# Kernel optimization log

Hardware: AMD Instinct MI355X
Metric: run time of the kernel (lower is better)

Reference implementation:

```python
import jax, jax.numpy as jnp
import numpy as np

B, N0, C, K, D = 16384, 1024, 12, 64, 3  # batch, feat dim, num_classes, num_clusters, ndim


def setup_inputs() -> dict:
    key = jax.random.key(0)
    ks = jax.random.split(key, 6)
    s = 0.02  # weight init scale
    return {
        "x": jax.random.normal(ks[0], (B, N0), dtype=jnp.float32),
        "Wfc": jax.random.normal(ks[1], (N0, C), dtype=jnp.float32) * s,
        "bfc": jnp.zeros((C,), dtype=jnp.float32),
        "Wbin": jax.random.normal(ks[2], (C, K, N0), dtype=jnp.float32) * s,
        "bbin": jnp.zeros((C, K), dtype=jnp.float32),
        "Wres": jax.random.normal(ks[3], (C, K, N0, D), dtype=jnp.float32) * s,
        "bres": jnp.zeros((C, K, D), dtype=jnp.float32),
        "centers": jax.random.normal(ks[4], (K, D), dtype=jnp.float32),
    }


def reference(x, Wfc, bfc, Wbin, bbin, Wres, bres, centers):
    # category head
    y0 = x @ Wfc + bfc                                            # [B, C]
    # per-class bin logits (batched over all classes at once)
    ybin = jnp.einsum("bn,ckn->bck", x, Wbin) + bbin              # [B, C, K]
    ind = jnp.argmax(ybin, axis=2)                                # [B, C] selected cluster per class
    # multires path: all (class, cluster) expert residuals, then one-hot select
    yres_all = jnp.einsum("bn,cknd->bckd", x, Wres) + bres        # [B, C, K, D]
    yres = jnp.take_along_axis(
        yres_all, ind[:, :, None, None], axis=2
    ).squeeze(2)                                                  # [B, C, D]
    # gather cluster centers and add residual
    y = centers[ind] + yres                                       # [B, C, D]
    # torch: stack over classes -> [C,B,D]; permute(1,2,0) -> [B, D, C]
    y1 = jnp.transpose(y, (0, 2, 1))                              # [B, D, C]
    return (y0, y1)
```

## Files before the change

### kernel.cpp

```cpp
#include <hip/hip_runtime.h>

typedef unsigned int uint32;
typedef unsigned long long uint64;
typedef unsigned short ushort16;
typedef __attribute__((ext_vector_type(8))) short bf16x8;
typedef __attribute__((ext_vector_type(4))) float f32x4;
typedef __attribute__((ext_vector_type(4))) uint32 u32x4;

#define B_SZ 16384
#define MARGIN 0.012f

__device__ __forceinline__ ushort16 f2bf(float f) {
  uint32 u = __float_as_uint(f);
  u += 0x7fffu + ((u >> 16) & 1u);
  return (ushort16)(u >> 16);
}
__device__ __forceinline__ float bf2f(ushort16 h) { return __uint_as_float(((uint32)h) << 16); }
__device__ __forceinline__ float bflo(uint32 u) { return __uint_as_float(u << 16); }
__device__ __forceinline__ float bfhi(uint32 u) { return __uint_as_float(u & 0xffff0000u); }
__device__ __forceinline__ uint32 pk2(float lo, float hi) {
  return ((uint32)f2bf(hi) << 16) | (uint32)f2bf(lo);
}
__device__ __forceinline__ int dot4(uint32 a, uint32 b, int c) {
#if __has_builtin(__builtin_amdgcn_sdot4)
  return __builtin_amdgcn_sdot4((int)a, (int)b, c, false);
#else
  int s = c;
#pragma unroll
  for (int k = 0; k < 4; ++k)
    s += (int)(char)(a >> (8 * k)) * (int)(char)(b >> (8 * k));
  return s;
#endif
}
__device__ __forceinline__ int q8(float v, float inv) {
  int q = (int)rintf(v * inv);
  return q > 127 ? 127 : (q < -127 ? -127 : q);
}
__device__ __forceinline__ int red16_i(int s) {
  s += __builtin_amdgcn_update_dpp(0, s, 0xB1, 0xF, 0xF, true);
  s += __builtin_amdgcn_update_dpp(0, s, 0x4E, 0xF, 0xF, true);
  s += __builtin_amdgcn_update_dpp(0, s, 0x141, 0xF, 0xF, true);
  s += __builtin_amdgcn_update_dpp(0, s, 0x140, 0xF, 0xF, true);
  return s;
}
#define DPP_D_LEVEL(v, ctrl)                                                        \
  {                                                                                 \
    uint64 u_ = (uint64)__double_as_longlong(v);                                    \
    int lo_ = __builtin_amdgcn_update_dpp(0, (int)(uint32)u_, (ctrl), 0xF, 0xF, true); \
    int hi_ = __builtin_amdgcn_update_dpp(0, (int)(uint32)(u_ >> 32), (ctrl), 0xF, 0xF, true); \
    (v) += __longlong_as_double((long long)(((uint64)(uint32)hi_ << 32) | (uint32)lo_)); \
  }
__device__ __forceinline__ double red16_d(double v) {
  DPP_D_LEVEL(v, 0xB1); DPP_D_LEVEL(v, 0x4E);
  DPP_D_LEVEL(v, 0x141); DPP_D_LEVEL(v, 0x140);
  return v;
}

__global__ __launch_bounds__(256) void prep_all(
    const float* __restrict__ Wfc, const float* __restrict__ Wbin,
    const float* __restrict__ Wres, const float* __restrict__ x,
    ushort16* __restrict__ Wall, uint32* __restrict__ wq, float* __restrict__ swk,
    uint2* __restrict__ xb, uint32* __restrict__ xq, float* __restrict__ sxb) {
  __shared__ float red[256];
  const int blk = blockIdx.x;
  const int t = threadIdx.x;
  if (blk < 3584) {
    int idx = blk * 256 + t;
    int j = idx >> 10, n = idx & 1023;
    float v = 0.f;
    if (j < 12) v = Wfc[n * 12 + j];
    else if (j >= 64 && j < 832) v = Wbin[(size_t)(j - 64) * 1024 + n];
    Wall[idx] = f2bf(v);
  } else if (blk < 4352) {
    const int ck = blk - 3584;
    const float4* base4 = (const float4*)(Wres + (size_t)ck * 3072);
    float4 v0 = base4[3 * t], v1 = base4[3 * t + 1], v2 = base4[3 * t + 2];
    float vals[12] = {v0.x, v0.y, v0.z, v0.w, v1.x, v1.y, v1.z, v1.w, v2.x, v2.y, v2.z, v2.w};
    float m = 0.f;
#pragma unroll
    for (int i = 0; i < 12; ++i) m = fmaxf(m, fabsf(vals[i]));
    red[t] = m; __syncthreads();
    for (int s = 128; s; s >>= 1) { if (t < s) red[t] = fmaxf(red[t], red[t + s]); __syncthreads(); }
    float mx = fmaxf(red[0], 1e-20f);
    float inv = 127.f / mx;
    if (t == 0) swk[ck] = mx / 127.f;
#pragma unroll
    for (int d = 0; d < 3; ++d) {
      uint32 u = 0;
#pragma unroll
      for (int j = 0; j < 4; ++j)
        u |= ((uint32)(unsigned char)(char)q8(vals[j * 3 + d], inv)) << (8 * j);
      wq[((size_t)(ck * 3 + d) << 8) + t] = u;
    }
  } else {
    const int lane = t & 63;
    const int b = (blk - 4352) * 4 + (t >> 6);
    const float4* xr = (const float4*)(x + (size_t)b * 1024 + lane * 16);
    float4 v0 = xr[0], v1 = xr[1], v2 = xr[2], v3 = xr[3];
    float xv[16] = {v0.x, v0.y, v0.z, v0.w, v1.x, v1.y, v1.z, v1.w,
                    v2.x, v2.y, v2.z, v2.w, v3.x, v3.y, v3.z, v3.w};
    u32x4 pa, pb;
    pa.x = pk2(xv[0], xv[1]);  pa.y = pk2(xv[2], xv[3]);
    pa.z = pk2(xv[4], xv[5]);  pa.w = pk2(xv[6], xv[7]);
    pb.x = pk2(xv[8], xv[9]);  pb.y = pk2(xv[10], xv[11]);
    pb.z = pk2(xv[12], xv[13]); pb.w = pk2(xv[14], xv[15]);
    u32x4* xbrow = (u32x4*)((uint32*)xb + (size_t)b * 512);
    xbrow[2 * lane] = pa;
    xbrow[2 * lane + 1] = pb;
    float m = 0.f;
#pragma unroll
    for (int i = 0; i < 16; ++i) m = fmaxf(m, fabsf(xv[i]));
    for (int off = 32; off; off >>= 1) m = fmaxf(m, __shfl_xor(m, off));
    float mx = fmaxf(m, 1e-20f);
    float inv = 127.f / mx;
    if (lane == 0) sxb[b] = mx / 127.f;
    u32x4 qv;
#pragma unroll
    for (int q = 0; q < 4; ++q) {
      uint32 u = ((uint32)(unsigned char)(char)q8(xv[4 * q + 0], inv)) |
                 ((uint32)(unsigned char)(char)q8(xv[4 * q + 1], inv)) << 8 |
                 ((uint32)(unsigned char)(char)q8(xv[4 * q + 2], inv)) << 16 |
                 ((uint32)(unsigned char)(char)q8(xv[4 * q + 3], inv)) << 24;
      qv[q] = u;
    }
    ((u32x4*)(xq + (size_t)b * 256))[lane] = qv;
  }
}

__global__ void prep_wall_f(const float* __restrict__ Wfc, const float* __restrict__ Wbin,
                            ushort16* __restrict__ Wall) {
  int idx = blockIdx.x * 256 + threadIdx.x;
  int j = idx >> 10, n = idx & 1023;
  float v = 0.f;
  if (j < 12) v = Wfc[n * 12 + j];
  else if (j >= 64 && j < 832) v = Wbin[(size_t)(j - 64) * 1024 + n];
  Wall[idx] = f2bf(v);
}
__global__ void prep_wres(const float* __restrict__ Wres, ushort16* __restrict__ Wres_b) {
  int idx = blockIdx.x * 256 + threadIdx.x;
  int n = idx & 1023;
  int d = (idx >> 10) % 3;
  int ck = idx / 3072;
  Wres_b[idx] = f2bf(Wres[((size_t)ck * 1024 + n) * 3 + d]);
}

template<int XB>
__global__ __launch_bounds__(256) void gemm_mfma(
    const float* __restrict__ x, const ushort16* __restrict__ xb,
    const float* __restrict__ bfc, const float* __restrict__ bbin,
    const ushort16* __restrict__ Wall, ushort16* __restrict__ ybin,
    unsigned char* __restrict__ ind8, uint64* __restrict__ mask64,
    float* __restrict__ out) {
  __shared__ __align__(16) char smem[65536];
  const int t = threadIdx.x;
  const int lane = t & 63, wid = t >> 6;
  const int wm = wid & 1, wn = wid >> 1;

  int orig = blockIdx.x;
  int bid = (orig & 7) * 112 + (orig >> 3);
  int nb = bid % 7, mb = bid / 7;
  const int b0 = mb * 128;

  f32x4 acc[4][4];
#pragma unroll
  for (int i = 0; i < 4; ++i)
#pragma unroll
    for (int j = 0; j < 4; ++j) acc[i][j] = (f32x4){0.f, 0.f, 0.f, 0.f};

  const int lr = lane & 15, lq = lane >> 4;

#define GLDS(srcp, dstoff)                                                      \
  __builtin_amdgcn_global_load_lds(                                             \
      (const __attribute__((address_space(1))) uint32*)(srcp),                  \
      (__attribute__((address_space(3))) uint32*)(smem + (dstoff)), 16, 0, 0)

  if (XB) {
    const int gs2 = (lane & 3) ^ ((lane >> 2) & 3);
    const int grw2 = lane >> 2;
    const int ch0 = wid * 2, ch1 = wid * 2 + 1;
    const ushort16* arow0 = xb + (size_t)(b0 + ch0 * 16 + grw2) * 1024 + gs2 * 8;
    const ushort16* arow1 = xb + (size_t)(b0 + ch1 * 16 + grw2) * 1024 + gs2 * 8;
    const ushort16* brow0 = Wall + (size_t)(nb * 128 + ch0 * 16 + grw2) * 1024 + gs2 * 8;
    const ushort16* brow1 = Wall + (size_t)(nb * 128 + ch1 * 16 + grw2) * 1024 + gs2 * 8;

#define STAGE_HALF(h)                                                           \
    {                                                                           \
      int bb_ = ((h) & 3) * 16384;                                              \
      int kc_ = (h) * 32;                                                       \
      GLDS(arow0 + kc_, bb_ + ch0 * 1024);                                      \
      GLDS(arow1 + kc_, bb_ + ch1 * 1024);                                      \
      GLDS(brow0 + kc_, bb_ + 8192 + ch0 * 1024);                               \
      GLDS(brow1 + kc_, bb_ + 8192 + ch1 * 1024);                               \
    }

    STAGE_HALF(0); STAGE_HALF(1); STAGE_HALF(2);
    const int cbx2 = (lq * 16) ^ ((lr & 3) << 4);
    const int arow_off = (wm * 64 + lr) * 64;
    const int brow_off = (wn * 64 + lr) * 64;
#pragma unroll 1
    for (int h = 0; h < 32; ++h) {
      if (h < 30)      asm volatile("s_waitcnt vmcnt(8)" ::: "memory");
      else if (h == 30) asm volatile("s_waitcnt vmcnt(4)" ::: "memory");
      else              asm volatile("s_waitcnt vmcnt(0)" ::: "memory");
      __builtin_amdgcn_s_barrier();
      if (h < 29) STAGE_HALF(h + 3);
      const char* base = smem + (h & 3) * 16384;
      bf16x8 af[4], bfr[4];
#pragma unroll
      for (int i = 0; i < 4; ++i)
        af[i] = *(const bf16x8*)(base + arow_off + i * 1024 + cbx2);
#pragma unroll
      for (int j = 0; j < 4; ++j)
        bfr[j] = *(const bf16x8*)(base + 8192 + brow_off + j * 1024 + cbx2);
#pragma unroll
      for (int i = 0; i < 4; ++i)
#pragma unroll
        for (int j = 0; j < 4; ++j)
          acc[i][j] = __builtin_amdgcn_mfma_f32_16x16x32_bf16(af[i], bfr[j], acc[i][j], 0, 0, 0);
    }
#undef STAGE_HALF
  } else {
    const int fxor = (lr & 7) << 4;
    for (int kc = 0; kc < 1024; kc += 64) {
      __syncthreads();
      const int sxor = ((t >> 3) & 7) << 4;
#pragma unroll
      for (int i = 0; i < 4; ++i) {
        int s = t + i * 256;
        int row = s >> 3, c8 = (s & 7) * 8;
        int dst = row * 128 + ((c8 * 2) ^ sxor);
        const float4* src = (const float4*)(x + (size_t)(b0 + row) * 1024 + kc + c8);
        float4 v0 = src[0], v1 = src[1];
        u32x4 pv;
        pv.x = pk2(v0.x, v0.y); pv.y = pk2(v0.z, v0.w);
        pv.z = pk2(v1.x, v1.y); pv.w = pk2(v1.z, v1.w);
        *(u32x4*)(smem + dst) = pv;
      }
#pragma unroll
      for (int i = 0; i < 4; ++i) {
        int s = t + i * 256;
        int row = s >> 3, c8 = (s & 7) * 8;
        int dst = 16384 + row * 128 + ((c8 * 2) ^ sxor);
        u32x4 v = *(const u32x4*)(Wall + (size_t)(nb * 128 + row) * 1024 + kc + c8);
        *(u32x4*)(smem + dst) = v;
      }
      __syncthreads();
#pragma unroll
      for (int kk = 0; kk < 2; ++kk) {
        int cbx = (kk * 64 + lq * 16) ^ fxor;
        bf16x8 af[4], bfr[4];
#pragma unroll
        for (int i = 0; i < 4; ++i)
          af[i] = *(const bf16x8*)(smem + (wm * 64 + i * 16 + lr) * 128 + cbx);
#pragma unroll
        for (int j = 0; j < 4; ++j)
          bfr[j] = *(const bf16x8*)(smem + 16384 + (wn * 64 + j * 16 + lr) * 128 + cbx);
#pragma unroll
        for (int i = 0; i < 4; ++i)
#pragma unroll
          for (int j = 0; j < 4; ++j)
            acc[i][j] = __builtin_amdgcn_mfma_f32_16x16x32_bf16(af[i], bfr[j], acc[i][j], 0, 0, 0);
      }
    }
  }
#undef GLDS

  const int g = 2 * nb + wn;
  if (g == 0) {
#pragma unroll
    for (int i = 0; i < 4; ++i)
#pragma unroll
      for (int r = 0; r < 4; ++r) {
        int gm = b0 + wm * 64 + i * 16 + lq * 4 + r;
        if (lr < 12) out[(size_t)gm * 12 + lr] = acc[i][0][r] + bfc[lr];
      }
    return;
  }
  if (g > 12) return;
  const int c = g - 1;
  if (XB == 0) {
#pragma unroll
    for (int i = 0; i < 4; ++i)
#pragma unroll
      for (int j = 0; j < 4; ++j)
#pragma unroll
        for (int r = 0; r < 4; ++r) {
          int gm = b0 + wm * 64 + i * 16 + lq * 4 + r;
          int col = j * 16 + lr;
          ybin[((size_t)gm * 12 + c) * 64 + col] = f2bf(acc[i][j][r] + bbin[c * 64 + col]);
        }
    return;
  }
  float bb[4];
#pragma unroll
  for (int j = 0; j < 4; ++j) bb[j] = bbin[c * 64 + j * 16 + lr];
#pragma unroll
  for (int i = 0; i < 4; ++i)
#pragma unroll
    for (int r = 0; r < 4; ++r) {
      float v0 = acc[i][0][r] + bb[0], v1 = acc[i][1][r] + bb[1];
      float v2 = acc[i][2][r] + bb[2], v3 = acc[i][3][r] + bb[3];
      float m1 = v0, m2 = -3.4e38f; int k1 = lr;
      if (v1 > m1) { m2 = m1; m1 = v1; k1 = 16 + lr; } else m2 = fmaxf(m2, v1);
      if (v2 > m1) { m2 = m1; m1 = v2; k1 = 32 + lr; } else m2 = fmaxf(m2, v2);
      if (v3 > m1) { m2 = m1; m1 = v3; k1 = 48 + lr; } else m2 = fmaxf(m2, v3);
#pragma unroll
      for (int off = 1; off < 16; off <<= 1) {
        float om1 = __shfl_xor(m1, off);
        int   ok1 = __shfl_xor(k1, off);
        float om2 = __shfl_xor(m2, off);
        bool take = (om1 > m1) || (om1 == m1 && ok1 < k1);
        float lose = take ? m1 : om1;
        m2 = fmaxf(fmaxf(m2, om2), lose);
        if (take) { m1 = om1; k1 = ok1; }
      }
      float thr = m1 - MARGIN;
      uint64 bl0 = __ballot(v0 >= thr);
      uint64 bl1 = __ballot(v1 >= thr);
      uint64 bl2 = __ballot(v2 >= thr);
      uint64 bl3 = __ballot(v3 >= thr);
      if (lr == 0) {
        int row = wm * 64 + i * 16 + lq * 4 + r;
        uint64 mk = ((bl0 >> (lq * 16)) & 0xffffull) |
                    (((bl1 >> (lq * 16)) & 0xffffull) << 16) |
                    (((bl2 >> (lq * 16)) & 0xffffull) << 32) |
                    (((bl3 >> (lq * 16)) & 0xffffull) << 48);
        int gp = (b0 + row) * 12 + c;
        ind8[gp] = (unsigned char)(k1 | ((m1 - m2 <= MARGIN) ? 128 : 0));
        mask64[gp] = mk;
      }
    }
}

__global__ __launch_bounds__(256) void compact_k(const unsigned char* __restrict__ ind8,
                                                 uint32* __restrict__ cnt,
                                                 uint32* __restrict__ wl) {
  const int b = blockIdx.x * 256 + threadIdx.x;
  const int lane = threadIdx.x & 63;
  const uint32* p = (const uint32*)(ind8 + b * 12);
  uint32 d0 = p[0], d1 = p[1], d2 = p[2];
  uint32 fmask = 0;
#pragma unroll
  for (int j = 0; j < 4; ++j) {
    if ((d0 >> (8 * j)) & 128u) fmask |= 1u << j;
    if ((d1 >> (8 * j)) & 128u) fmask |= 1u << (4 + j);
    if ((d2 >> (8 * j)) & 128u) fmask |= 1u << (8 + j);
  }
  uint32 n_i = (uint32)__popc(fmask);
  uint32 pre = n_i;
  for (int off = 1; off < 64; off <<= 1) {
    uint32 v = __shfl_up(pre, off);
    if (lane >= off) pre += v;
  }
  uint32 total = __shfl(pre, 63);
  uint32 base = 0;
  if (lane == 63 && total) base = atomicAdd(cnt, total);
  base = __shfl(base, 63);
  uint32 off = base + pre - n_i;
  while (fmask) {
    int c = __ffs(fmask) - 1;
    fmask &= fmask - 1;
    wl[off++] = (uint32)(b * 12 + c);
  }
}

__global__ __launch_bounds__(256) void tail_k(
    const float* __restrict__ x, const float* __restrict__ Wbin,
    const float* __restrict__ bbin, const float* __restrict__ bres,
    const float* __restrict__ centers, const unsigned char* __restrict__ ind8,
    const uint64* __restrict__ mask64, const uint32* __restrict__ wq,
    const float* __restrict__ swk, const uint32* __restrict__ xq,
    const float* __restrict__ sxb, const uint32* __restrict__ cnt,
    const uint32* __restrict__ wl, float* __restrict__ out) {
  const int lane = threadIdx.x & 63;
  const int w = threadIdx.x >> 6;
  const int rm = (int)(blockIdx.x % 3u);
  const int rq = (int)(blockIdx.x / 3u);

  if (rm == 0) {
    const uint32 nresc = *cnt;
#pragma unroll 1
    for (uint32 slot = rq * 4 + w; slot < nresc; slot += 32768) {
      const uint32 pp = wl[slot];
      const int b = (int)(pp / 12u), c = (int)(pp % 12u);

      float xv[16];
      const float4* xr = (const float4*)(x + (size_t)b * 1024 + lane * 16);
#pragma unroll
      for (int q = 0; q < 4; ++q) {
        float4 vv = xr[q];
        xv[4 * q] = vv.x; xv[4 * q + 1] = vv.y; xv[4 * q + 2] = vv.z; xv[4 * q + 3] = vv.w;
      }
      const float sx = sxb[b];
      const float inv = (sx > 0.f) ? 1.f / sx : 0.f;
      uint32 xi[4];
#pragma unroll
      for (int q = 0; q < 4; ++q)
        xi[q] = ((uint32)(unsigned char)(char)q8(xv[4 * q + 0], inv)) |
                ((uint32)(unsigned char)(char)q8(xv[4 * q + 1], inv)) << 8 |
                ((uint32)(unsigned char)(char)q8(xv[4 * q + 2], inv)) << 16 |
                ((uint32)(unsigned char)(char)q8(xv[4 * q + 3], inv)) << 24;

      uint64 mask = mask64[pp];
      double best = -1.0e300;
      int bk = 0;
#pragma unroll 1
      while (mask) {
        int kk[4];
        int nc = 0;
        while (mask && nc < 4) { kk[nc++] = __ffsll(mask) - 1; mask &= mask - 1; }
#pragma unroll
        for (int j = 1; j < 4; ++j) if (j >= nc) kk[j] = kk[0];
        double s[4] = {0.0, 0.0, 0.0, 0.0};
#pragma unroll
        for (int ci = 0; ci < 4; ++ci) {
          const float4* wr4 = (const float4*)(Wbin + ((size_t)c * 64 + kk[ci]) * 1024 + lane * 16);
#pragma unroll
          for (int q = 0; q < 4; ++q) {
            float4 wvv = wr4[q];
            s[ci] += (double)xv[4 * q] * (double)wvv.x + (double)xv[4 * q + 1] * (double)wvv.y +
                     (double)xv[4 * q + 2] * (double)wvv.z + (double)xv[4 * q + 3] * (double)wvv.w;
          }
        }
#pragma unroll
        for (int ci = 0; ci < 4; ++ci) s[ci] = red16_d(s[ci]);
        for (int off = 16; off < 64; off <<= 1) {
#pragma unroll
          for (int ci = 0; ci < 4; ++ci) s[ci] += __shfl_xor(s[ci], off);
        }
#pragma unroll
        for (int ci = 0; ci < 4; ++ci) {
          double sv = s[ci] + (double)bbin[c * 64 + kk[ci]];
          if (ci < nc && sv > best) { best = sv; bk = kk[ci]; }
        }
      }
      const int ck = c * 64 + bk;
      const uint32* wr = wq + (size_t)ck * 768;
      int acc[3];
#pragma unroll
      for (int d = 0; d < 3; ++d) {
        u32x4 wvq = *(const u32x4*)(wr + d * 256 + lane * 4);
        int ss = dot4(xi[0], wvq.x, 0);
        ss = dot4(xi[1], wvq.y, ss);
        ss = dot4(xi[2], wvq.z, ss);
        acc[d] = dot4(xi[3], wvq.w, ss);
      }
#pragma unroll
      for (int d = 0; d < 3; ++d) acc[d] = red16_i(acc[d]);
      for (int off = 16; off < 64; off <<= 1) {
        acc[0] += __shfl_xor(acc[0], off);
        acc[1] += __shfl_xor(acc[1], off);
        acc[2] += __shfl_xor(acc[2], off);
      }
      if (lane == 0) {
        const size_t obase = (size_t)B_SZ * 12 + (size_t)b * 36;
        float sc = sx * swk[ck];
        out[obase + 0 * 12 + c] = centers[bk * 3 + 0] + bres[ck * 3 + 0] + sc * (float)acc[0];
        out[obase + 1 * 12 + c] = centers[bk * 3 + 1] + bres[ck * 3 + 1] + sc * (float)acc[1];
        out[obase + 2 * 12 + c] = centers[bk * 3 + 2] + bres[ck * 3 + 2] + sc * (float)acc[2];
      }
    }
    return;
  }

  const int b = rq * 2 + (rm - 1);

  const u32x4 xi = *(const u32x4*)(xq + (size_t)b * 256 + lane * 4);
  const float sx = sxb[b];
  const size_t obase = (size_t)B_SZ * 12 + (size_t)b * 36;

  int iv[3], ind[3], ck[3];
  u32x4 wv[3][3];
#pragma unroll
  for (int cc = 0; cc < 3; ++cc) {
    int c = w * 3 + cc;
    iv[cc] = ind8[b * 12 + c];
    ind[cc] = iv[cc] & 63;
    ck[cc] = c * 64 + ind[cc];
    const uint32* wr = wq + (size_t)ck[cc] * 768;
#pragma unroll
    for (int d = 0; d < 3; ++d)
      wv[cc][d] = *(const u32x4*)(wr + d * 256 + lane * 4);
  }
  int acc[3][3];
#pragma unroll
  for (int cc = 0; cc < 3; ++cc)
#pragma unroll
    for (int d = 0; d < 3; ++d) {
      int s = dot4(xi.x, wv[cc][d].x, 0);
      s = dot4(xi.y, wv[cc][d].y, s);
      s = dot4(xi.z, wv[cc][d].z, s);
      acc[cc][d] = dot4(xi.w, wv[cc][d].w, s);
    }
#pragma unroll
  for (int cc = 0; cc < 3; ++cc)
#pragma unroll
    for (int d = 0; d < 3; ++d)
      acc[cc][d] = red16_i(acc[cc][d]);
  for (int off = 16; off < 64; off <<= 1) {
#pragma unroll
    for (int cc = 0; cc < 3; ++cc)
#pragma unroll
      for (int d = 0; d < 3; ++d)
        acc[cc][d] += __shfl_xor(acc[cc][d], off);
  }
  if (lane == 0) {
#pragma unroll
    for (int cc = 0; cc < 3; ++cc) {
      if (iv[cc] & 128) continue;
      int c = w * 3 + cc;
      float sc = sx * swk[ck[cc]];
      out[obase + 0 * 12 + c] = centers[ind[cc] * 3 + 0] + bres[ck[cc] * 3 + 0] + sc * (float)acc[cc][0];
      out[obase + 1 * 12 + c] = centers[ind[cc] * 3 + 1] + bres[ck[cc] * 3 + 1] + sc * (float)acc[cc][1];
      out[obase + 2 * 12 + c] = centers[ind[cc] * 3 + 2] + bres[ck[cc] * 3 + 2] + sc * (float)acc[cc][2];
    }
  }
}

__global__ __launch_bounds__(256) void select2(
    const float* __restrict__ x, const float* __restrict__ Wbin,
    const float* __restrict__ bbin, const float* __restrict__ bres,
    const float* __restrict__ centers, const ushort16* __restrict__ Wres_b,
    const ushort16* __restrict__ ybin, float* __restrict__ out) {
  const int lane = threadIdx.x & 63;
  const int w = threadIdx.x >> 6;
  const int b = blockIdx.x;
  float xv[16];
  {
    const float4* xr = (const float4*)(x + (size_t)b * 1024 + lane * 16);
#pragma unroll
    for (int q = 0; q < 4; ++q) {
      float4 v = xr[q];
      xv[4 * q] = v.x; xv[4 * q + 1] = v.y; xv[4 * q + 2] = v.z; xv[4 * q + 3] = v.w;
    }
  }
  const size_t obase = (size_t)B_SZ * 12 + (size_t)b * 36;
#pragma unroll 1
  for (int cc = 0; cc < 3; ++cc) {
    const int c = w * 3 + cc;
    float v = bf2f(ybin[((size_t)b * 12 + c) * 64 + lane]);
    float m1 = v, m2 = -3.4e38f;
    int k1 = lane;
    for (int off = 32; off; off >>= 1) {
      float om1 = __shfl_xor(m1, off);
      int   ok1 = __shfl_xor(k1, off);
      float om2 = __shfl_xor(m2, off);
      bool take = (om1 > m1) || (om1 == m1 && ok1 < k1);
      float lose = take ? m1 : om1;
      m2 = fmaxf(fmaxf(m2, om2), lose);
      if (take) { m1 = om1; k1 = ok1; }
    }
    int ind = k1;
    if (m1 - m2 <= MARGIN) {
      unsigned long long mask = __ballot(v >= m1 - MARGIN);
      double best = -1.0e300;
      int bk = 0;
      while (mask) {
        int k = __ffsll(mask) - 1;
        mask &= (mask - 1);
        const float4* wr4 = (const float4*)(Wbin + ((size_t)c * 64 + k) * 1024 + lane * 16);
        double s = 0.0;
#pragma unroll
        for (int q = 0; q < 4; ++q) {
          float4 wv = wr4[q];
          s += (double)xv[4 * q] * (double)wv.x + (double)xv[4 * q + 1] * (double)wv.y +
               (double)xv[4 * q + 2] * (double)wv.z + (double)xv[4 * q + 3] * (double)wv.w;
        }
        for (int off = 32; off; off >>= 1) s += __shfl_xor(s, off);
        s += (double)bbin[c * 64 + k];
        if (s > best) { best = s; bk = k; }
      }
      ind = bk;
    }
    const ushort16* wr = Wres_b + ((size_t)(c * 64 + ind) * 3) * 1024;
    float a[3] = {0.f, 0.f, 0.f};
#pragma unroll
    for (int d = 0; d < 3; ++d) {
      const u32x4* pp = (const u32x4*)(wr + d * 1024 + lane * 16);
      u32x4 w0 = pp[0], w1 = pp[1];
      uint32 uw[8] = {w0.x, w0.y, w0.z, w0.w, w1.x, w1.y, w1.z, w1.w};
#pragma unroll
      for (int q = 0; q < 8; ++q) {
        a[d] = fmaf(xv[2 * q],     bflo(uw[q]), a[d]);
        a[d] = fmaf(xv[2 * q + 1], bfhi(uw[q]), a[d]);
      }
    }
    for (int off = 32; off; off >>= 1) {
      a[0] += __shfl_xor(a[0], off);
      a[1] += __shfl_xor(a[1], off);
      a[2] += __shfl_xor(a[2], off);
    }
    if (lane == 0) {
      int ck = c * 64 + ind;
      out[obase + 0 * 12 + c] = centers[ind * 3 + 0] + bres[ck * 3 + 0] + a[0];
      out[obase + 1 * 12 + c] = centers[ind * 3 + 1] + bres[ck * 3 + 1] + a[1];
      out[obase + 2 * 12 + c] = centers[ind * 3 + 2] + bres[ck * 3 + 2] + a[2];
    }
  }
}

extern "C" void kernel_launch(void* const* d_in, const int* in_sizes, int n_in,
                              void* d_out, int out_size, void* d_ws, size_t ws_size,
                              hipStream_t stream) {
  const float* x       = (const float*)d_in[0];
  const float* Wfc     = (const float*)d_in[1];
  const float* bfc     = (const float*)d_in[2];
  const float* Wbin    = (const float*)d_in[3];
  const float* bbin    = (const float*)d_in[4];
  const float* Wres    = (const float*)d_in[5];
  const float* bres    = (const float*)d_in[6];
  const float* centers = (const float*)d_in[7];
  float* out = (float*)d_out;

  char* ws = (char*)d_ws;
  ushort16* Wall = (ushort16*)ws;
  if (ws_size >= 57151488ull) {
    uint32*        wq     = (uint32*)(ws + 1835008);
    float*         swk    = (float*)(ws + 4194304);
    unsigned char* ind8   = (unsigned char*)(ws + 4197376);
    uint64*        mask64 = (uint64*)(ws + 4393984);
    ushort16*      xb     = (ushort16*)(ws + 5966848);
    uint32*        xq     = (uint32*)(ws + 39521280);
    float*         sxb    = (float*)(ws + 56298496);
    uint32*        cnt    = (uint32*)(ws + 56364032);
    uint32*        wl     = (uint32*)(ws + 56364288);

    hipMemsetAsync(cnt, 0, 4, stream);
    prep_all<<<8448, 256, 0, stream>>>(Wfc, Wbin, Wres, x, Wall, wq, swk,
                                       (uint2*)xb, xq, sxb);
    gemm_mfma<1><<<896, 256, 0, stream>>>(x, xb, bfc, bbin, Wall,
                                          (ushort16*)nullptr, ind8, mask64, out);
    compact_k<<<64, 256, 0, stream>>>(ind8, cnt, wl);
    tail_k<<<24576, 256, 0, stream>>>(x, Wbin, bbin, bres, centers, ind8, mask64,
                                      wq, swk, xq, sxb, cnt, wl, out);
  } else {
    ushort16* Wres_b = (ushort16*)(ws + 1835008);
    ushort16* ybin   = (ushort16*)(ws + 6553600);
    prep_wall_f<<<3584, 256, 0, stream>>>(Wfc, Wbin, Wall);
    prep_wres<<<9216, 256, 0, stream>>>(Wres, Wres_b);
    gemm_mfma<0><<<896, 256, 0, stream>>>(x, (const ushort16*)ws, bfc, bbin, Wall,
                                          ybin, (unsigned char*)nullptr,
                                          (uint64*)nullptr, out);
    select2<<<B_SZ, 256, 0, stream>>>(x, Wbin, bbin, bres, centers, Wres_b, ybin, out);
  }
}
```

Baseline: 145.8 us.

## Move Wres quantization into GEMM launch and use triple-buffered LDS pipeline

The Wres int8 quantization blocks move out of the prep kernel and run as extra blocks (768) appended to the GEMM launch, so that work can overlap with GEMM tiles. The GEMM's LDS staging drops from four buffers to three (64KB to 48KB shared memory), with a prefetch distance of two stages instead of three. The aim is better occupancy and overlap. In exchange there is less latency hiding per block.

```diff
diff --git a/kernel.cpp b/kernel.cpp
--- a/kernel.cpp
+++ b/kernel.cpp
@@ -58,10 +58,8 @@
 
 __global__ __launch_bounds__(256) void prep_all(
     const float* __restrict__ Wfc, const float* __restrict__ Wbin,
-    const float* __restrict__ Wres, const float* __restrict__ x,
-    ushort16* __restrict__ Wall, uint32* __restrict__ wq, float* __restrict__ swk,
+    const float* __restrict__ x, ushort16* __restrict__ Wall,
     uint2* __restrict__ xb, uint32* __restrict__ xq, float* __restrict__ sxb) {
-  __shared__ float red[256];
   const int blk = blockIdx.x;
   const int t = threadIdx.x;
   if (blk < 3584) {
@@ -71,30 +69,9 @@
     if (j < 12) v = Wfc[n * 12 + j];
     else if (j >= 64 && j < 832) v = Wbin[(size_t)(j - 64) * 1024 + n];
     Wall[idx] = f2bf(v);
-  } else if (blk < 4352) {
-    const int ck = blk - 3584;
-    const float4* base4 = (const float4*)(Wres + (size_t)ck * 3072);
-    float4 v0 = base4[3 * t], v1 = base4[3 * t + 1], v2 = base4[3 * t + 2];
-    float vals[12] = {v0.x, v0.y, v0.z, v0.w, v1.x, v1.y, v1.z, v1.w, v2.x, v2.y, v2.z, v2.w};
-    float m = 0.f;
-#pragma unroll
-    for (int i = 0; i < 12; ++i) m = fmaxf(m, fabsf(vals[i]));
-    red[t] = m; __syncthreads();
-    for (int s = 128; s; s >>= 1) { if (t < s) red[t] = fmaxf(red[t], red[t + s]); __syncthreads(); }
-    float mx = fmaxf(red[0], 1e-20f);
-    float inv = 127.f / mx;
-    if (t == 0) swk[ck] = mx / 127.f;
-#pragma unroll
-    for (int d = 0; d < 3; ++d) {
-      uint32 u = 0;
-#pragma unroll
-      for (int j = 0; j < 4; ++j)
-        u |= ((uint32)(unsigned char)(char)q8(vals[j * 3 + d], inv)) << (8 * j);
-      wq[((size_t)(ck * 3 + d) << 8) + t] = u;
-    }
   } else {
     const int lane = t & 63;
-    const int b = (blk - 4352) * 4 + (t >> 6);
+    const int b = (blk - 3584) * 4 + (t >> 6);
     const float4* xr = (const float4*)(x + (size_t)b * 1024 + lane * 16);
     float4 v0 = xr[0], v1 = xr[1], v2 = xr[2], v3 = xr[3];
     float xv[16] = {v0.x, v0.y, v0.z, v0.w, v1.x, v1.y, v1.z, v1.w,
@@ -150,9 +127,36 @@
     const float* __restrict__ bfc, const float* __restrict__ bbin,
     const ushort16* __restrict__ Wall, ushort16* __restrict__ ybin,
     unsigned char* __restrict__ ind8, uint64* __restrict__ mask64,
-    float* __restrict__ out) {
-  __shared__ __align__(16) char smem[65536];
+    const float* __restrict__ Wres, uint32* __restrict__ wq,
+    float* __restrict__ swk, float* __restrict__ out) {
+  __shared__ __align__(16) char smem[49152];
   const int t = threadIdx.x;
+
+  if (XB && blockIdx.x >= 896) {
+    float* red = (float*)smem;
+    const int ck = blockIdx.x - 896;
+    const float4* base4 = (const float4*)(Wres + (size_t)ck * 3072);
+    float4 v0 = base4[3 * t], v1 = base4[3 * t + 1], v2 = base4[3 * t + 2];
+    float vals[12] = {v0.x, v0.y, v0.z, v0.w, v1.x, v1.y, v1.z, v1.w, v2.x, v2.y, v2.z, v2.w};
+    float m = 0.f;
+#pragma unroll
+    for (int i = 0; i < 12; ++i) m = fmaxf(m, fabsf(vals[i]));
+    red[t] = m; __syncthreads();
+    for (int s = 128; s; s >>= 1) { if (t < s) red[t] = fmaxf(red[t], red[t + s]); __syncthreads(); }
+    float mx = fmaxf(red[0], 1e-20f);
+    float inv = 127.f / mx;
+    if (t == 0) swk[ck] = mx / 127.f;
+#pragma unroll
+    for (int d = 0; d < 3; ++d) {
+      uint32 u = 0;
+#pragma unroll
+      for (int j = 0; j < 4; ++j)
+        u |= ((uint32)(unsigned char)(char)q8(vals[j * 3 + d], inv)) << (8 * j);
+      wq[((size_t)(ck * 3 + d) << 8) + t] = u;
+    }
+    return;
+  }
+
   const int lane = t & 63, wid = t >> 6;
   const int wm = wid & 1, wn = wid >> 1;
 
@@ -183,9 +187,9 @@
     const ushort16* brow0 = Wall + (size_t)(nb * 128 + ch0 * 16 + grw2) * 1024 + gs2 * 8;
     const ushort16* brow1 = Wall + (size_t)(nb * 128 + ch1 * 16 + grw2) * 1024 + gs2 * 8;
 
-#define STAGE_HALF(h)                                                           \
+#define STAGE_HALF(h, buf)                                                      \
     {                                                                           \
-      int bb_ = ((h) & 3) * 16384;                                              \
+      int bb_ = (buf) * 16384;                                                  \
       int kc_ = (h) * 32;                                                       \
       GLDS(arow0 + kc_, bb_ + ch0 * 1024);                                      \
       GLDS(arow1 + kc_, bb_ + ch1 * 1024);                                      \
@@ -193,18 +197,21 @@
       GLDS(brow1 + kc_, bb_ + 8192 + ch1 * 1024);                               \
     }
 
-    STAGE_HALF(0); STAGE_HALF(1); STAGE_HALF(2);
+    STAGE_HALF(0, 0); STAGE_HALF(1, 1);
     const int cbx2 = (lq * 16) ^ ((lr & 3) << 4);
     const int arow_off = (wm * 64 + lr) * 64;
     const int brow_off = (wn * 64 + lr) * 64;
+    int rb = 0;
 #pragma unroll 1
     for (int h = 0; h < 32; ++h) {
-      if (h < 30)      asm volatile("s_waitcnt vmcnt(8)" ::: "memory");
-      else if (h == 30) asm volatile("s_waitcnt vmcnt(4)" ::: "memory");
-      else              asm volatile("s_waitcnt vmcnt(0)" ::: "memory");
+      if (h < 31) asm volatile("s_waitcnt vmcnt(4)" ::: "memory");
+      else        asm volatile("s_waitcnt vmcnt(0)" ::: "memory");
       __builtin_amdgcn_s_barrier();
-      if (h < 29) STAGE_HALF(h + 3);
-      const char* base = smem + (h & 3) * 16384;
+      if (h < 30) {
+        int sb = rb + 2; if (sb >= 3) sb -= 3;
+        STAGE_HALF(h + 2, sb);
+      }
+      const char* base = smem + rb * 16384;
       bf16x8 af[4], bfr[4];
 #pragma unroll
       for (int i = 0; i < 4; ++i)
@@ -217,6 +224,7 @@
 #pragma unroll
         for (int j = 0; j < 4; ++j)
           acc[i][j] = __builtin_amdgcn_mfma_f32_16x16x32_bf16(af[i], bfr[j], acc[i][j], 0, 0, 0);
+      rb = (rb == 2) ? 0 : rb + 1;
     }
 #undef STAGE_HALF
   } else {
@@ -626,10 +634,10 @@
     uint32*        wl     = (uint32*)(ws + 56364288);
 
     hipMemsetAsync(cnt, 0, 4, stream);
-    prep_all<<<8448, 256, 0, stream>>>(Wfc, Wbin, Wres, x, Wall, wq, swk,
-                                       (uint2*)xb, xq, sxb);
-    gemm_mfma<1><<<896, 256, 0, stream>>>(x, xb, bfc, bbin, Wall,
-                                          (ushort16*)nullptr, ind8, mask64, out);
+    prep_all<<<7680, 256, 0, stream>>>(Wfc, Wbin, x, Wall, (uint2*)xb, xq, sxb);
+    gemm_mfma<1><<<1664, 256, 0, stream>>>(x, xb, bfc, bbin, Wall,
+                                           (ushort16*)nullptr, ind8, mask64,
+                                           Wres, wq, swk, out);
     compact_k<<<64, 256, 0, stream>>>(ind8, cnt, wl);
     tail_k<<<24576, 256, 0, stream>>>(x, Wbin, bbin, bres, centers, ind8, mask64,
                                       wq, swk, xq, sxb, cnt, wl, out);
@@ -640,7 +648,8 @@
     prep_wres<<<9216, 256, 0, stream>>>(Wres, Wres_b);
     gemm_mfma<0><<<896, 256, 0, stream>>>(x, (const ushort16*)ws, bfc, bbin, Wall,
                                           ybin, (unsigned char*)nullptr,
-                                          (uint64*)nullptr, out);
+                                          (uint64*)nullptr, nullptr,
+                                          (uint32*)nullptr, (float*)nullptr, out);
     select2<<<B_SZ, 256, 0, stream>>>(x, Wbin, bbin, bres, centers, Wres_b, ybin, out);
   }
 }
```

New measurement: 143.3 us. About the same (-1.7%).
